# Kernel optimization log

Hardware: AMD Instinct MI355X
Metric: run time of the kernel (lower is better)

The kernel has to match this reference:

```python
import jax, jax.numpy as jnp
import numpy as np

B = 4096
N0 = 784          # MNIST input
L0 = 263          # fc0: Gather chain 784 -> 256 (ELU after each)
L2 = 121          # fc2: Gather chain 256 -> 12 (ELU after each); final Gather 12 -> 10 has no ELU


def _win3(x):
    # x: (B, N) -> (B, N-2, 3) sliding windows of width 3
    return jnp.stack([x[:, :-2], x[:, 1:-1], x[:, 2:]], axis=-1)


def setup_inputs() -> dict:
    key = jax.random.key(0)
    kx, k0, k1, k2, k3, k4 = jax.random.split(key, 6)
    s = 0.75  # keeps activation variance roughly stable through ~380 ELU glia layers
    x = jax.random.normal(kx, (B, N0), jnp.float32)
    W0 = jax.random.normal(k0, (L0, 782, 3), jnp.float32) * s
    m0 = np.arange(782)[None, :] < (780 - 2 * np.arange(L0))[:, None]
    W0 = W0 * jnp.asarray(m0[..., None], jnp.float32)  # zero out rows past each layer's out size
    Ws = jax.random.normal(k1, (256, 3), jnp.float32) * s
    bs = jax.random.normal(k2, (256,), jnp.float32) * 0.1
    W2 = jax.random.normal(k3, (L2, 254, 3), jnp.float32) * s
    m2 = np.arange(254)[None, :] < (252 - 2 * np.arange(L2))[:, None]
    W2 = W2 * jnp.asarray(m2[..., None], jnp.float32)
    Wlast = jax.random.normal(k4, (10, 3), jnp.float32) * s
    return {"x": x, "W0": W0, "Ws": Ws, "bs": bs, "W2": W2, "Wlast": Wlast}


def reference(x, W0, Ws, bs, W2, Wlast):
    def gather_step(h, W):
        # locally-connected width-3 Gather (out = in - 2, bias=False) + ELU.
        # Invalid tail rows of W are zero, so padded positions stay exactly 0
        # (ELU(0)=0) and never contaminate valid windows.
        y = jax.nn.elu(jnp.einsum('bjk,jk->bj', _win3(h), W))
        return jnp.pad(y, ((0, 0), (0, 2))), None

    # fc0: 263 Gather+ELU layers, 784 -> 256 (valid prefix of fixed-width state)
    h, _ = jax.lax.scan(gather_step, x, W0)
    h = h[:, :256]
    # fc1: Slide(256) + ELU -- same-size width-3 locally connected layer, zero-padded window, bias
    hp = jnp.pad(h, ((0, 0), (1, 1)))
    h = jax.nn.elu(jnp.einsum('bjk,jk->bj', _win3(hp), Ws) + bs)
    # fc2: 121 Gather+ELU layers, 256 -> 12
    h, _ = jax.lax.scan(gather_step, h, W2)
    # final Gather(12): 12 -> 10, no ELU
    logits = jnp.einsum('bjk,jk->bj', _win3(h[:, :12]), Wlast)
    return jax.nn.log_softmax(logits, axis=1)
```

## Files before the change

### kernel.cpp

```cpp
#include <hip/hip_runtime.h>
#include <math.h>


#define G 2

__device__ __forceinline__ float elu_f(float a) {
    return a > 0.0f ? a : (__expf(a) - 1.0f);
}

template<int N>
__device__ __forceinline__ void load_w(float (&w)[N], const float* __restrict__ p) {
#pragma unroll
    for (int j = 0; j < N; ++j) w[j] = p[j];
}

template<int K>
__device__ __forceinline__ void scan_layer(float (&h)[K], const float (&w)[3 * K]) {
    float e0 = __shfl_down(h[0], 1);
    float e1;
    if constexpr (K >= 2) e1 = __shfl_down(h[1], 1);
    else                  e1 = __shfl_down(h[0], 2);
#pragma unroll
    for (int i = 0; i < K; ++i) {
        float x1 = (i + 1 < K) ? h[i + 1] : e0;
        float x2 = (i + 2 < K) ? h[i + 2] : ((i + 2 == K) ? e0 : e1);
        float a = fmaf(h[i], w[3 * i], fmaf(x1, w[3 * i + 1], x2 * w[3 * i + 2]));
        h[i] = elu_f(a);
    }
}

template<int K>
__device__ __forceinline__ void scan_phase(const float* __restrict__ W, int lstride,
                                           int l0, int l1, int lane,
                                           float (&hA)[K], float (&hB)[K]) {
    int base = 3 * K * lane;
    if (base + 3 * K > lstride) base = lstride - 3 * K;
    const float* __restrict__ Wp = W + (size_t)l0 * lstride + base;
    float wa[3 * K], wb[3 * K];
    load_w(wa, Wp);
    int l = l0;
    for (; l + 2 <= l1; l += 2) {
        load_w(wb, Wp + lstride);
        scan_layer<K>(hA, wa);
        scan_layer<K>(hB, wa);
        if (l + 3 <= l1) load_w(wa, Wp + 2 * (size_t)lstride);
        scan_layer<K>(hA, wb);
        scan_layer<K>(hB, wb);
        Wp += 2 * (size_t)lstride;
    }
    if (l < l1) { scan_layer<K>(hA, wa); scan_layer<K>(hB, wa); }
}

template<int KA, int KB>
__device__ __forceinline__ void repack2(float (&aA)[KA], float (&aB)[KA],
                                        float (&nA)[KB], float (&nB)[KB],
                                        float* lds, int lane) {
    __syncthreads();
#pragma unroll
    for (int i = 0; i < KA; ++i) lds[KA * lane + i] = aA[i];
    __syncthreads();
#pragma unroll
    for (int i = 0; i < KB; ++i) nA[i] = lds[KB * lane + i];
    __syncthreads();
#pragma unroll
    for (int i = 0; i < KA; ++i) lds[KA * lane + i] = aB[i];
    __syncthreads();
#pragma unroll
    for (int i = 0; i < KB; ++i) nB[i] = lds[KB * lane + i];
    __syncthreads();
}

__device__ __forceinline__ void stage2(float (&hA)[5], float (&hB)[5],
                                       const float* __restrict__ Ws,
                                       const float* __restrict__ bs, int lane) {
#pragma unroll
    for (int i = 0; i < 5; ++i) {
        if (5 * lane + i > 255) { hA[i] = 0.0f; hB[i] = 0.0f; }
    }
    float w[15], bb[5];
#pragma unroll
    for (int i = 0; i < 5; ++i) {
        int j = 5 * lane + i;
        bool v = j < 256;
        w[3 * i + 0] = v ? Ws[3 * j + 0] : 0.0f;
        w[3 * i + 1] = v ? Ws[3 * j + 1] : 0.0f;
        w[3 * i + 2] = v ? Ws[3 * j + 2] : 0.0f;
        bb[i]        = v ? bs[j]         : 0.0f;
    }
    float pA = __shfl_up(hA[4], 1); if (lane == 0) pA = 0.0f;
    float pB = __shfl_up(hB[4], 1); if (lane == 0) pB = 0.0f;
    float qA = __shfl_down(hA[0], 1);
    float qB = __shfl_down(hB[0], 1);
    float yA[5], yB[5];
#pragma unroll
    for (int i = 0; i < 5; ++i) {
        float xmA = (i == 0) ? pA : hA[i - 1];
        float xpA = (i == 4) ? qA : hA[i + 1];
        yA[i] = elu_f(fmaf(xmA, w[3 * i], fmaf(hA[i], w[3 * i + 1], fmaf(xpA, w[3 * i + 2], bb[i]))));
        float xmB = (i == 0) ? pB : hB[i - 1];
        float xpB = (i == 4) ? qB : hB[i + 1];
        yB[i] = elu_f(fmaf(xmB, w[3 * i], fmaf(hB[i], w[3 * i + 1], fmaf(xpB, w[3 * i + 2], bb[i]))));
    }
#pragma unroll
    for (int i = 0; i < 5; ++i) { hA[i] = yA[i]; hB[i] = yB[i]; }
}

__device__ __forceinline__ void emit_row(float v, const float* __restrict__ Wl,
                                         float* __restrict__ out, int row, int lane) {
    float n1 = __shfl_down(v, 1);
    float n2 = __shfl_down(v, 2);
    float lg = 0.0f;
    if (lane < 10)
        lg = fmaf(v, Wl[3 * lane], fmaf(n1, Wl[3 * lane + 1], n2 * Wl[3 * lane + 2]));
    float t = (lane < 10) ? lg : -1e30f;
#pragma unroll
    for (int d = 1; d < 16; d <<= 1) t = fmaxf(t, __shfl_xor(t, d));
    float e = (lane < 10) ? __expf(lg - t) : 0.0f;
    float s = e;
#pragma unroll
    for (int d = 1; d < 16; d <<= 1) s += __shfl_xor(s, d);
    float lse = t + __logf(s);
    if (lane < 10) out[(size_t)row * 10 + lane] = lg - lse;
}

__global__ __launch_bounds__(64)
void pg_kernel(const float* __restrict__ x,  const float* __restrict__ W0,
               const float* __restrict__ Ws, const float* __restrict__ bs,
               const float* __restrict__ W2, const float* __restrict__ Wlast,
               float* __restrict__ out)
{
    __shared__ float lds[13 * 64];
    const int lane = threadIdx.x;
    const int rowA = blockIdx.x * G;
    const int rowB = rowA + 1;

    float a13[13], b13[13];
#pragma unroll
    for (int i = 0; i < 13; ++i) {
        int p = 13 * lane + i;
        a13[i] = (p < 784) ? x[(size_t)rowA * 784 + p] : 0.0f;
        b13[i] = (p < 784) ? x[(size_t)rowB * 784 + p] : 0.0f;
    }

    scan_phase<13>(W0, 2346, 0, 71, lane, a13, b13);
    float a10[10], b10[10]; repack2<13, 10>(a13, b13, a10, b10, lds, lane);
    scan_phase<10>(W0, 2346, 71, 167, lane, a10, b10);
    float a7[7], b7[7];     repack2<10, 7>(a10, b10, a7, b7, lds, lane);
    scan_phase<7>(W0, 2346, 167, 231, lane, a7, b7);
    float a5[5], b5[5];     repack2<7, 5>(a7, b7, a5, b5, lds, lane);
    scan_phase<5>(W0, 2346, 231, 263, lane, a5, b5);

    stage2(a5, b5, Ws, bs, lane);

    float a4[4], b4[4];     repack2<5, 4>(a5, b5, a4, b4, lds, lane);
    scan_phase<4>(W2, 762, 0, 31, lane, a4, b4);
    float a3[3], b3[3];     repack2<4, 3>(a4, b4, a3, b3, lds, lane);
    scan_phase<3>(W2, 762, 31, 63, lane, a3, b3);
    float a2_[2], b2_[2];   repack2<3, 2>(a3, b3, a2_, b2_, lds, lane);
    scan_phase<2>(W2, 762, 63, 95, lane, a2_, b2_);
    float a1[1], b1[1];     repack2<2, 1>(a2_, b2_, a1, b1, lds, lane);
    scan_phase<1>(W2, 762, 95, 121, lane, a1, b1);

    emit_row(a1[0], Wlast, out, rowA, lane);
    emit_row(b1[0], Wlast, out, rowB, lane);
}

extern "C" void kernel_launch(void* const* d_in, const int* in_sizes, int n_in,
                              void* d_out, int out_size, void* d_ws, size_t ws_size,
                              hipStream_t stream) {
    const float* x     = (const float*)d_in[0];
    const float* W0    = (const float*)d_in[1];
    const float* Ws    = (const float*)d_in[2];
    const float* bs    = (const float*)d_in[3];
    const float* W2    = (const float*)d_in[4];
    const float* Wlast = (const float*)d_in[5];
    float* out = (float*)d_out;

    dim3 grid(4096 / G);
    dim3 block(64);
    pg_kernel<<<grid, block, 0, stream>>>(x, W0, Ws, bs, W2, Wlast, out);
}
```

Measured before the change: 264.2 us.

## Pre-transpose gather weights into lane-interleaved float4 layout for coalesced loads

Adds a preprocessing kernel that rewrites the W0 and W2 weight tensors into a per-phase, per-layer layout where each lane's weights sit in interleaved float4 chunks. The main kernel then loads weights with coalesced 16-byte vector loads instead of strided scalar loads at stride 3K per lane. The reorder runs on every call and costs an extra launch plus a pass over the weights; it needs workspace and falls back to the old kernel when none is available.

```diff
diff --git a/kernel.cpp b/kernel.cpp
--- a/kernel.cpp
+++ b/kernel.cpp
@@ -4,6 +4,8 @@
 
 #define G 2
 
+#define T_TOTAL 580864
+
 __device__ __forceinline__ float elu_f(float a) {
     return a > 0.0f ? a : (__expf(a) - 1.0f);
 }
@@ -14,8 +16,9 @@
     for (int j = 0; j < N; ++j) w[j] = p[j];
 }
 
-template<int K>
-__device__ __forceinline__ void scan_layer(float (&h)[K], const float (&w)[3 * K]) {
+template<int K, int NW>
+__device__ __forceinline__ void scan_layer(float (&h)[K], const float (&w)[NW]) {
+    static_assert(NW >= 3 * K, "weight array too small");
     float e0 = __shfl_down(h[0], 1);
     float e1;
     if constexpr (K >= 2) e1 = __shfl_down(h[1], 1);
@@ -27,6 +30,33 @@
         float a = fmaf(h[i], w[3 * i], fmaf(x1, w[3 * i + 1], x2 * w[3 * i + 2]));
         h[i] = elu_f(a);
     }
+}
+
+template<int NC, int NW>
+__device__ __forceinline__ void load_wt(float (&w)[NW], const float4* __restrict__ Tp, int lr) {
+#pragma unroll
+    for (int c = 0; c < NC; ++c) {
+        float4 v = Tp[(size_t)lr * (NC * 64) + c * 64];
+        w[4 * c + 0] = v.x; w[4 * c + 1] = v.y; w[4 * c + 2] = v.z; w[4 * c + 3] = v.w;
+    }
+}
+
+template<int K, int NC>
+__device__ __forceinline__ void scan_phase_t(const float* __restrict__ Tphase, int nl,
+                                             int lane, float (&hA)[K], float (&hB)[K]) {
+    const float4* __restrict__ Tp = reinterpret_cast<const float4*>(Tphase) + lane;
+    float wa[4 * NC], wb[4 * NC];
+    load_wt<NC>(wa, Tp, 0);
+    int l = 0;
+    for (; l + 2 <= nl; l += 2) {
+        load_wt<NC>(wb, Tp, l + 1);
+        scan_layer<K>(hA, wa);
+        scan_layer<K>(hB, wa);
+        if (l + 3 <= nl) load_wt<NC>(wa, Tp, l + 2);
+        scan_layer<K>(hA, wb);
+        scan_layer<K>(hB, wb);
+    }
+    if (l < nl) { scan_layer<K>(hA, wa); scan_layer<K>(hB, wa); }
 }
 
 template<int K>
@@ -123,11 +153,83 @@
     if (lane < 10) out[(size_t)row * 10 + lane] = lg - lse;
 }
 
+__global__ __launch_bounds__(256)
+void reorder_w(const float* __restrict__ W0, const float* __restrict__ W2,
+               float* __restrict__ T) {
+    int idx = blockIdx.x * 256 + threadIdx.x;
+    if (idx >= T_TOTAL) return;
+    int base, l0, K, NC, lstride; const float* Wsrc;
+    if      (idx < 181760) { base = 0;      l0 = 0;   K = 13; NC = 10; Wsrc = W0; lstride = 2346; }
+    else if (idx < 378368) { base = 181760; l0 = 71;  K = 10; NC = 8;  Wsrc = W0; lstride = 2346; }
+    else if (idx < 476672) { base = 378368; l0 = 167; K = 7;  NC = 6;  Wsrc = W0; lstride = 2346; }
+    else if (idx < 509440) { base = 476672; l0 = 231; K = 5;  NC = 4;  Wsrc = W0; lstride = 2346; }
+    else if (idx < 533248) { base = 509440; l0 = 0;   K = 4;  NC = 3;  Wsrc = W2; lstride = 762;  }
+    else if (idx < 557824) { base = 533248; l0 = 31;  K = 3;  NC = 3;  Wsrc = W2; lstride = 762;  }
+    else if (idx < 574208) { base = 557824; l0 = 63;  K = 2;  NC = 2;  Wsrc = W2; lstride = 762;  }
+    else                   { base = 574208; l0 = 95;  K = 1;  NC = 1;  Wsrc = W2; lstride = 762;  }
+    int rel  = idx - base;
+    int perL = NC * 256;
+    int lr   = rel / perL;
+    int r2   = rel - lr * perL;
+    int c    = r2 >> 8;
+    int ln   = (r2 >> 2) & 63;
+    int f    = r2 & 3;
+    int elem = 4 * c + f;
+    float v = 0.0f;
+    if (elem < 3 * K) {
+        int b = 3 * K * ln;
+        if (b + 3 * K > lstride) b = lstride - 3 * K;
+        v = Wsrc[(size_t)(l0 + lr) * lstride + b + elem];
+    }
+    T[idx] = v;
+}
+
 __global__ __launch_bounds__(64)
-void pg_kernel(const float* __restrict__ x,  const float* __restrict__ W0,
-               const float* __restrict__ Ws, const float* __restrict__ bs,
-               const float* __restrict__ W2, const float* __restrict__ Wlast,
-               float* __restrict__ out)
+void pg_kernel_t(const float* __restrict__ x,  const float* __restrict__ Ws,
+                 const float* __restrict__ bs, const float* __restrict__ Wlast,
+                 const float* __restrict__ T,  float* __restrict__ out)
+{
+    __shared__ float lds[13 * 64];
+    const int lane = threadIdx.x;
+    const int rowA = blockIdx.x * G;
+    const int rowB = rowA + 1;
+
+    float a13[13], b13[13];
+#pragma unroll
+    for (int i = 0; i < 13; ++i) {
+        int p = 13 * lane + i;
+        a13[i] = (p < 784) ? x[(size_t)rowA * 784 + p] : 0.0f;
+        b13[i] = (p < 784) ? x[(size_t)rowB * 784 + p] : 0.0f;
+    }
+
+    scan_phase_t<13, 10>(T + 0,      71, lane, a13, b13);
+    float a10[10], b10[10]; repack2<13, 10>(a13, b13, a10, b10, lds, lane);
+    scan_phase_t<10, 8>(T + 181760,  96, lane, a10, b10);
+    float a7[7], b7[7];     repack2<10, 7>(a10, b10, a7, b7, lds, lane);
+    scan_phase_t<7, 6>(T + 378368,   64, lane, a7, b7);
+    float a5[5], b5[5];     repack2<7, 5>(a7, b7, a5, b5, lds, lane);
+    scan_phase_t<5, 4>(T + 476672,   32, lane, a5, b5);
+
+    stage2(a5, b5, Ws, bs, lane);
+
+    float a4[4], b4[4];     repack2<5, 4>(a5, b5, a4, b4, lds, lane);
+    scan_phase_t<4, 3>(T + 509440,   31, lane, a4, b4);
+    float a3[3], b3[3];     repack2<4, 3>(a4, b4, a3, b3, lds, lane);
+    scan_phase_t<3, 3>(T + 533248,   32, lane, a3, b3);
+    float a2_[2], b2_[2];   repack2<3, 2>(a3, b3, a2_, b2_, lds, lane);
+    scan_phase_t<2, 2>(T + 557824,   32, lane, a2_, b2_);
+    float a1[1], b1[1];     repack2<2, 1>(a2_, b2_, a1, b1, lds, lane);
+    scan_phase_t<1, 1>(T + 574208,   26, lane, a1, b1);
+
+    emit_row(a1[0], Wlast, out, rowA, lane);
+    emit_row(b1[0], Wlast, out, rowB, lane);
+}
+
+__global__ __launch_bounds__(64)
+void pg_kernel_d(const float* __restrict__ x,  const float* __restrict__ W0,
+                 const float* __restrict__ Ws, const float* __restrict__ bs,
+                 const float* __restrict__ W2, const float* __restrict__ Wlast,
+                 float* __restrict__ out)
 {
     __shared__ float lds[13 * 64];
     const int lane = threadIdx.x;
@@ -176,7 +278,11 @@
     const float* Wlast = (const float*)d_in[5];
     float* out = (float*)d_out;
 
-    dim3 grid(4096 / G);
-    dim3 block(64);
-    pg_kernel<<<grid, block, 0, stream>>>(x, W0, Ws, bs, W2, Wlast, out);
-}
+    if (ws_size >= (size_t)T_TOTAL * sizeof(float)) {
+        float* T = (float*)d_ws;
+        reorder_w<<<(T_TOTAL + 255) / 256, 256, 0, stream>>>(W0, W2, T);
+        pg_kernel_t<<<4096 / G, 64, 0, stream>>>(x, Ws, bs, Wlast, T, out);
+    } else {
+        pg_kernel_d<<<4096 / G, 64, 0, stream>>>(x, W0, Ws, bs, W2, Wlast, out);
+    }
+}
```

Result: faster. 258.9 us (-2.0%).
